# Optimization experiments

Measured on AMD Instinct MI355X. Metric: run time of the kernel, lower is better.

## Reference

```python
import jax, jax.numpy as jnp
import numpy as np

NUM_HEADS = 8
DIM_HEAD = 128
SCALE = DIM_HEAD ** -0.5


def setup_inputs() -> dict:
    key = jax.random.key(0)
    ks = jax.random.split(key, 6)
    B, N, D = 8, 1024, 1024
    return {
        "s_v": jax.random.normal(ks[0], (B, N, D), jnp.float32),
        "s_m": jax.random.normal(ks[1], (B, N, D), jnp.float32),
        "g_l": jax.random.normal(ks[2], (B, NUM_HEADS, N, N), jnp.float32),
        "W_qkv": jax.random.normal(ks[3], (D, 3 * NUM_HEADS * DIM_HEAD), jnp.float32) * (D ** -0.5),
        "W_qk": jax.random.normal(ks[4], (D, 2 * NUM_HEADS * DIM_HEAD), jnp.float32) * (D ** -0.5),
        "W_out": jax.random.normal(ks[5], (NUM_HEADS * DIM_HEAD, D), jnp.float32) * ((NUM_HEADS * DIM_HEAD) ** -0.5),
        "b_out": jnp.zeros((D,), jnp.float32),
    }


def _split_heads(t):
    # [b, n, h*d] -> [b, h, n, d]
    b, n, hd = t.shape
    return t.reshape(b, n, NUM_HEADS, DIM_HEAD).transpose(0, 2, 1, 3)


def reference(s_v, s_m, g_l, W_qkv, W_qk, W_out, b_out):
    b, n, _ = s_v.shape
    q_v, k_v, v = [_split_heads(t) for t in jnp.split(s_v @ W_qkv, 3, axis=-1)]
    q_m, k_m = [_split_heads(t) for t in jnp.split(s_m @ W_qk, 2, axis=-1)]
    # trajectory attention probs (softmaxed) times raw value-stream scores
    p_m = jax.nn.softmax(jnp.einsum('bhid,bhjd->bhij', q_m, k_m), axis=-1)
    p_v = jnp.einsum('bhid,bhjd->bhij', q_v, k_v)
    dots = p_m * p_v * SCALE + g_l
    attn = jax.nn.softmax(dots, axis=-1)
    out = jnp.einsum('bhij,bhjd->bhid', attn, v)
    out = out.transpose(0, 2, 1, 3).reshape(b, n, NUM_HEADS * DIM_HEAD)
    return out @ W_out + b_out
```

## Files before the change

kernel.cpp:

```cpp
#include <hip/hip_runtime.h>

typedef __attribute__((ext_vector_type(8))) short short8;
typedef __attribute__((ext_vector_type(8))) unsigned short ushortx8;
typedef __attribute__((ext_vector_type(4))) unsigned short ushortx4;
typedef __attribute__((ext_vector_type(4))) float floatx4;

#define SCALE_F 0.08838834764831845f

__device__ __forceinline__ float b2f(unsigned short u) {
  union { unsigned int u; float f; } c; c.u = ((unsigned int)u) << 16; return c.f;
}
__device__ __forceinline__ unsigned short f2b(float f) {
  union { float f; unsigned int u; } c; c.f = f;
  unsigned int u = c.u;
  u += 0x7fffu + ((u >> 16) & 1u);
  return (unsigned short)(u >> 16);
}

#define GLD_LDS16(g, l)                                              \
  __builtin_amdgcn_global_load_lds(                                  \
      (const __attribute__((address_space(1))) void*)(g),            \
      (__attribute__((address_space(3))) void*)(l), 16, 0, 0)

__global__ __launch_bounds__(256) void cast_bf16_kernel(
    const float* __restrict__ x, unsigned short* __restrict__ y, int n) {
  int i = (blockIdx.x * 256 + threadIdx.x) * 4;
  if (i >= n) return;
  float4 v = *(const float4*)(x + i);
  ushortx4 o;
  o[0] = f2b(v.x); o[1] = f2b(v.y); o[2] = f2b(v.z); o[3] = f2b(v.w);
  *(ushortx4*)(y + i) = o;
}

__global__ __launch_bounds__(256) void split3_kernel(
    const float* __restrict__ x, unsigned short* __restrict__ y) {
  int idx = blockIdx.x * 256 + threadIdx.x;
  int row = idx >> 8;
  int c4 = (idx & 255) * 4;
  float4 v = *(const float4*)(x + (size_t)row * 1024 + c4);
  ushortx4 hi, lo;
  hi[0] = f2b(v.x); lo[0] = f2b(v.x - b2f(hi[0]));
  hi[1] = f2b(v.y); lo[1] = f2b(v.y - b2f(hi[1]));
  hi[2] = f2b(v.z); lo[2] = f2b(v.z - b2f(hi[2]));
  hi[3] = f2b(v.w); lo[3] = f2b(v.w - b2f(hi[3]));
  unsigned short* yr = y + (size_t)row * 3072;
  *(ushortx4*)(yr + c4) = hi;
  *(ushortx4*)(yr + 1024 + c4) = lo;
  *(ushortx4*)(yr + 2048 + c4) = hi;
}

__global__ __launch_bounds__(256) void transpose_split_qk(
    const float* __restrict__ W, unsigned short* __restrict__ y) {
  __shared__ float tile[32][33];
  int t = threadIdx.x, tx = t & 31, ty = t >> 5;
  int n0 = blockIdx.x * 32, k0 = blockIdx.y * 32;
  for (int rr = ty; rr < 32; rr += 8)
    tile[rr][tx] = W[(size_t)(k0 + rr) * 2048 + n0 + tx];
  __syncthreads();
  for (int rr = ty; rr < 32; rr += 8) {
    float v = tile[tx][rr];
    unsigned short hi = f2b(v);
    unsigned short lo = f2b(v - b2f(hi));
    unsigned short* yr = y + (size_t)(n0 + rr) * 3072;
    yr[k0 + tx] = hi;
    yr[1024 + k0 + tx] = hi;
    yr[2048 + k0 + tx] = lo;
  }
}

template<int MODE>
__global__ __launch_bounds__(256) void transpose_any(
    const void* __restrict__ inv, void* __restrict__ outv,
    int R, int C, int ldin, int ldout,
    long sIb, long sIh, long sOb, long sOh, int pstart) {
  int z = blockIdx.z, p = pstart + z, b = p >> 3, h = p & 7;
  size_t ioff = (size_t)(sIb * b + sIh * h);
  size_t ooff = (size_t)(sOb * b + sOh * h);
  __shared__ float tile[32][33];
  int t = threadIdx.x, tx = t & 31, ty = t >> 5;
  int c0 = blockIdx.x * 32, r0 = blockIdx.y * 32;
  for (int rr = ty; rr < 32; rr += 8) {
    size_t idx = ioff + (size_t)(r0 + rr) * ldin + (c0 + tx);
    tile[rr][tx] = (MODE == 2) ? b2f(((const unsigned short*)inv)[idx])
                               : ((const float*)inv)[idx];
  }
  __syncthreads();
  for (int rr = ty; rr < 32; rr += 8) {
    size_t idx = ooff + (size_t)(c0 + rr) * ldout + (r0 + tx);
    ((unsigned short*)outv)[idx] = f2b(tile[tx][rr]);
  }
}

template<int OUT_BF16, int ADD_BIAS>
__global__ __launch_bounds__(256) void gemm128(
    const unsigned short* __restrict__ A, const unsigned short* __restrict__ BT,
    void* __restrict__ Cv, const float* __restrict__ bias,
    int K, int lda, int ldb, int ldc,
    long sAz, long sAb, long sAh, long sBz, long sBb, long sBh,
    long sCz, long sCb, long sCh, int pstart) {
  int z = blockIdx.z, p = pstart + z, bb = p >> 3, hh = p & 7;
  A  += (size_t)(sAz * z + sAb * bb + sAh * hh);
  BT += (size_t)(sBz * z + sBb * bb + sBh * hh);
  size_t coff = (size_t)(sCz * z + sCb * bb + sCh * hh);

  __shared__ unsigned short Al[128][32];
  __shared__ unsigned short Bl[128][32];
  int t = threadIdx.x;
  int m0 = blockIdx.y * 128, n0 = blockIdx.x * 128;
  int w = t >> 6, l = t & 63;
  int wm = (w >> 1) * 64, wn = (w & 1) * 64;
  int lrow = l & 15, lq = l >> 4;
  floatx4 acc[4][4] = {};

  int srow = t >> 2, scol = (t & 3) * 8;
  const unsigned short* ga = A + (size_t)(m0 + srow) * lda + scol;
  const unsigned short* gb = BT + (size_t)(n0 + srow) * ldb + scol;
  unsigned short* la = &Al[srow][scol];
  unsigned short* lb = &Bl[srow][scol];
  size_t lda64 = (size_t)64 * lda, ldb64 = (size_t)64 * ldb;

  for (int k0 = 0; k0 < K; k0 += 32) {
    GLD_LDS16(ga + k0, la);
    GLD_LDS16(ga + lda64 + k0, la + 64 * 32);
    GLD_LDS16(gb + k0, lb);
    GLD_LDS16(gb + ldb64 + k0, lb + 64 * 32);
    __syncthreads();
    short8 af[4], bf[4];
#pragma unroll
    for (int i = 0; i < 4; i++) af[i] = *(const short8*)&Al[wm + i * 16 + lrow][lq * 8];
#pragma unroll
    for (int j = 0; j < 4; j++) bf[j] = *(const short8*)&Bl[wn + j * 16 + lrow][lq * 8];
#pragma unroll
    for (int i = 0; i < 4; i++)
#pragma unroll
      for (int j = 0; j < 4; j++)
        acc[i][j] = __builtin_amdgcn_mfma_f32_16x16x32_bf16(af[i], bf[j], acc[i][j], 0, 0, 0);
    __syncthreads();
  }
#pragma unroll
  for (int i = 0; i < 4; i++)
#pragma unroll
    for (int j = 0; j < 4; j++)
#pragma unroll
      for (int r = 0; r < 4; r++) {
        int row = m0 + wm + i * 16 + lq * 4 + r;
        int col = n0 + wn + j * 16 + lrow;
        float v = acc[i][j][r];
        if (ADD_BIAS) v += bias[col];
        size_t idx = coff + (size_t)row * ldc + col;
        if (OUT_BF16) ((unsigned short*)Cv)[idx] = f2b(v);
        else          ((float*)Cv)[idx] = v;
      }
}

__global__ __launch_bounds__(256) void logits_prep(
    const float* __restrict__ qkf, unsigned short* __restrict__ qm,
    unsigned short* __restrict__ km, int pstart) {
  int idx = blockIdx.x * 256 + threadIdx.x;
  int z = blockIdx.y;
  int i = idx >> 5;
  int d4 = (idx & 31) * 4;
  int p = pstart + z, b = p >> 3, h = p & 7;
  const float* row = qkf + ((size_t)(b * 1024 + i)) * 2048 + h * 128;
  ushortx4 hi, lo;

  float4 q = *(const float4*)(row + d4);
  hi[0] = f2b(q.x); lo[0] = f2b(q.x - b2f(hi[0]));
  hi[1] = f2b(q.y); lo[1] = f2b(q.y - b2f(hi[1]));
  hi[2] = f2b(q.z); lo[2] = f2b(q.z - b2f(hi[2]));
  hi[3] = f2b(q.w); lo[3] = f2b(q.w - b2f(hi[3]));
  unsigned short* qr = qm + ((size_t)z * 1024 + i) * 384;
  *(ushortx4*)(qr + d4) = hi;
  *(ushortx4*)(qr + 128 + d4) = lo;
  *(ushortx4*)(qr + 256 + d4) = hi;

  float4 k = *(const float4*)(row + 1024 + d4);
  hi[0] = f2b(k.x); lo[0] = f2b(k.x - b2f(hi[0]));
  hi[1] = f2b(k.y); lo[1] = f2b(k.y - b2f(hi[1]));
  hi[2] = f2b(k.z); lo[2] = f2b(k.z - b2f(hi[2]));
  hi[3] = f2b(k.w); lo[3] = f2b(k.w - b2f(hi[3]));
  unsigned short* kr = km + ((size_t)z * 1024 + i) * 384;
  *(ushortx4*)(kr + d4) = hi;
  *(ushortx4*)(kr + 128 + d4) = hi;
  *(ushortx4*)(kr + 256 + d4) = lo;
}

__global__ __launch_bounds__(256) void softmax_combine(
    const float* __restrict__ smb, unsigned short* __restrict__ pvb,
    const float* __restrict__ g_l, int pstart) {
  int i = blockIdx.x, z = blockIdx.y;
  int p = pstart + z;
  const float* srow = smb + ((size_t)z * 1024 + i) * 1024;
  unsigned short* vrow = pvb + ((size_t)z * 1024 + i) * 1024;
  const float* grow = g_l + ((size_t)p * 1024 + i) * 1024;
  int t = threadIdx.x;
  __shared__ float red[4];

  float4 s = *(const float4*)(srow + t * 4);
  float mx = fmaxf(fmaxf(s.x, s.y), fmaxf(s.z, s.w));
#pragma unroll
  for (int o = 32; o; o >>= 1) mx = fmaxf(mx, __shfl_xor(mx, o));
  if ((t & 63) == 0) red[t >> 6] = mx;
  __syncthreads();
  mx = fmaxf(fmaxf(red[0], red[1]), fmaxf(red[2], red[3]));
  __syncthreads();
  float4 e;
  e.x = __expf(s.x - mx); e.y = __expf(s.y - mx);
  e.z = __expf(s.z - mx); e.w = __expf(s.w - mx);
  float sum = e.x + e.y + e.z + e.w;
#pragma unroll
  for (int o = 32; o; o >>= 1) sum += __shfl_xor(sum, o);
  if ((t & 63) == 0) red[t >> 6] = sum;
  __syncthreads();
  float inv = 1.0f / (red[0] + red[1] + red[2] + red[3]);
  __syncthreads();

  ushortx4 pv = *(const ushortx4*)(vrow + t * 4);
  float4 g = *(const float4*)(grow + t * 4);
  float4 d;
  d.x = e.x * inv * b2f(pv[0]) * SCALE_F + g.x;
  d.y = e.y * inv * b2f(pv[1]) * SCALE_F + g.y;
  d.z = e.z * inv * b2f(pv[2]) * SCALE_F + g.z;
  d.w = e.w * inv * b2f(pv[3]) * SCALE_F + g.w;

  float mx2 = fmaxf(fmaxf(d.x, d.y), fmaxf(d.z, d.w));
#pragma unroll
  for (int o = 32; o; o >>= 1) mx2 = fmaxf(mx2, __shfl_xor(mx2, o));
  if ((t & 63) == 0) red[t >> 6] = mx2;
  __syncthreads();
  mx2 = fmaxf(fmaxf(red[0], red[1]), fmaxf(red[2], red[3]));
  __syncthreads();
  float4 e2;
  e2.x = __expf(d.x - mx2); e2.y = __expf(d.y - mx2);
  e2.z = __expf(d.z - mx2); e2.w = __expf(d.w - mx2);
  float sum2 = e2.x + e2.y + e2.z + e2.w;
#pragma unroll
  for (int o = 32; o; o >>= 1) sum2 += __shfl_xor(sum2, o);
  if ((t & 63) == 0) red[t >> 6] = sum2;
  __syncthreads();
  float inv2 = 1.0f / (red[0] + red[1] + red[2] + red[3]);

  ushortx4 o4;
  o4[0] = f2b(e2.x * inv2); o4[1] = f2b(e2.y * inv2);
  o4[2] = f2b(e2.z * inv2); o4[3] = f2b(e2.w * inv2);
  *(ushortx4*)(vrow + t * 4) = o4;
}

extern "C" void kernel_launch(void* const* d_in, const int* in_sizes, int n_in,
                              void* d_out, int out_size, void* d_ws, size_t ws_size,
                              hipStream_t stream) {
  (void)in_sizes; (void)n_in; (void)out_size; (void)ws_size;
  const float* s_v   = (const float*)d_in[0];
  const float* s_m   = (const float*)d_in[1];
  const float* g_l   = (const float*)d_in[2];
  const float* W_qkv = (const float*)d_in[3];
  const float* W_qk  = (const float*)d_in[4];
  const float* W_out = (const float*)d_in[5];
  const float* b_out = (const float*)d_in[6];
  float* out = (float*)d_out;
  char* ws = (char*)d_ws;

  unsigned short* sv_bf  = (unsigned short*)(ws);
  unsigned short* qm384  = (unsigned short*)(ws);
  unsigned short* wtqkv  = (unsigned short*)(ws + 16777216);
  unsigned short* km384  = (unsigned short*)(ws + 16777216);
  unsigned short* wtout  = (unsigned short*)(ws + 29360128);
  unsigned short* qkvb   = (unsigned short*)(ws + 31457280);
  float*          qkf    = (float*)(ws + 81788928);
  unsigned short* vt     = (unsigned short*)(ws + 148897792);
  unsigned short* ao     = (unsigned short*)(ws + 165675008);
  unsigned short* smhl   = (unsigned short*)(ws + 182452224);
  float*          smb    = (float*)(ws + 182452224);
  unsigned short* wqk_hl = (unsigned short*)(ws + 249561088);
  unsigned short* pvb    = (unsigned short*)(ws + 249561088);

  cast_bf16_kernel<<<dim3(8192), 256, 0, stream>>>(s_v, sv_bf, 8388608);
  transpose_any<0><<<dim3(96, 32, 1), 256, 0, stream>>>(
      W_qkv, wtqkv, 1024, 3072, 3072, 1024, 0, 0, 0, 0, 0);
  transpose_any<0><<<dim3(32, 32, 1), 256, 0, stream>>>(
      W_out, wtout, 1024, 1024, 1024, 1024, 0, 0, 0, 0, 0);
  split3_kernel<<<dim3(8192), 256, 0, stream>>>(s_m, smhl);
  transpose_split_qk<<<dim3(64, 32, 1), 256, 0, stream>>>(W_qk, wqk_hl);
  gemm128<1, 0><<<dim3(24, 64, 1), 256, 0, stream>>>(
      sv_bf, wtqkv, qkvb, nullptr, 1024, 1024, 1024, 3072,
      0, 0, 0, 0, 0, 0, 0, 0, 0, 0);
  gemm128<0, 0><<<dim3(16, 64, 1), 256, 0, stream>>>(
      smhl, wqk_hl, qkf, nullptr, 3072, 3072, 3072, 2048,
      0, 0, 0, 0, 0, 0, 0, 0, 0, 0);
  transpose_any<2><<<dim3(4, 32, 64), 256, 0, stream>>>(
      qkvb + 2048, vt, 1024, 128, 3072, 1024,
      (long)1024 * 3072, 128, (long)1048576, 131072, 0);

  for (int c = 0; c < 4; c++) {
    int pstart = c * 16;
    logits_prep<<<dim3(128, 16), 256, 0, stream>>>(qkf, qm384, km384, pstart);
    gemm128<0, 0><<<dim3(8, 8, 16), 256, 0, stream>>>(
        qm384, km384, smb, nullptr, 384, 384, 384, 1024,
        (long)1024 * 384, 0, 0, (long)1024 * 384, 0, 0,
        (long)1048576, 0, 0, pstart);
    gemm128<1, 0><<<dim3(8, 8, 16), 256, 0, stream>>>(
        qkvb, qkvb + 1024, pvb, nullptr, 128, 3072, 3072, 1024,
        0, (long)1024 * 3072, 128, 0, (long)1024 * 3072, 128,
        (long)1048576, 0, 0, pstart);
    softmax_combine<<<dim3(1024, 16), 256, 0, stream>>>(smb, pvb, g_l, pstart);
    gemm128<1, 0><<<dim3(1, 8, 16), 256, 0, stream>>>(
        pvb, vt, ao, nullptr, 1024, 1024, 1024, 1024,
        (long)1048576, 0, 0, 0, (long)1048576, 131072,
        0, (long)1048576, 128, pstart);
  }
  gemm128<0, 1><<<dim3(8, 64, 1), 256, 0, stream>>>(
      ao, wtout, out, b_out, 1024, 1024, 1024, 1024,
      0, 0, 0, 0, 0, 0, 0, 0, 0, 0);
}
```

Baseline: 1.140 ms.

## Fuse value-stream QK, combine softmax and PV into flash-style kernel

Replaces three stages per chunk (the q_v·k_v GEMM writing a bf16 score matrix, the two-pass softmax_combine, and the attn·V GEMM) with a row_stats kernel plus one fused attn_pv kernel. attn_pv computes q_v·k_v tiles with MFMA, applies the precomputed trajectory softmax stats, adds g_l, runs an online softmax and accumulates P·V in registers. This removes the pvb round-trip through memory. The cost is a small grid (32x16 blocks of 256 threads), many syncthreads, and uncoalesced scalar loads of smb and g_l, which may hurt occupancy and bandwidth.

New measurement: 1.219 ms. +7.0%, slower.

```diff
diff --git a/kernel.cpp b/kernel.cpp
--- a/kernel.cpp
+++ b/kernel.cpp
@@ -185,65 +185,197 @@
   *(ushortx4*)(kr + 256 + d4) = lo;
 }
 
-__global__ __launch_bounds__(256) void softmax_combine(
-    const float* __restrict__ smb, unsigned short* __restrict__ pvb,
-    const float* __restrict__ g_l, int pstart) {
-  int i = blockIdx.x, z = blockIdx.y;
-  int p = pstart + z;
-  const float* srow = smb + ((size_t)z * 1024 + i) * 1024;
-  unsigned short* vrow = pvb + ((size_t)z * 1024 + i) * 1024;
-  const float* grow = g_l + ((size_t)p * 1024 + i) * 1024;
-  int t = threadIdx.x;
+__global__ __launch_bounds__(256) void row_stats(
+    const float* __restrict__ smb, float* __restrict__ mlb) {
+  int row = blockIdx.x, z = blockIdx.y, t = threadIdx.x;
+  const float* sr = smb + ((size_t)z * 1024 + row) * 1024;
   __shared__ float red[4];
-
-  float4 s = *(const float4*)(srow + t * 4);
-  float mx = fmaxf(fmaxf(s.x, s.y), fmaxf(s.z, s.w));
+  float4 v = *(const float4*)(sr + t * 4);
+  float mx = fmaxf(fmaxf(v.x, v.y), fmaxf(v.z, v.w));
 #pragma unroll
   for (int o = 32; o; o >>= 1) mx = fmaxf(mx, __shfl_xor(mx, o));
   if ((t & 63) == 0) red[t >> 6] = mx;
   __syncthreads();
   mx = fmaxf(fmaxf(red[0], red[1]), fmaxf(red[2], red[3]));
   __syncthreads();
-  float4 e;
-  e.x = __expf(s.x - mx); e.y = __expf(s.y - mx);
-  e.z = __expf(s.z - mx); e.w = __expf(s.w - mx);
-  float sum = e.x + e.y + e.z + e.w;
-#pragma unroll
-  for (int o = 32; o; o >>= 1) sum += __shfl_xor(sum, o);
-  if ((t & 63) == 0) red[t >> 6] = sum;
-  __syncthreads();
-  float inv = 1.0f / (red[0] + red[1] + red[2] + red[3]);
-  __syncthreads();
-
-  ushortx4 pv = *(const ushortx4*)(vrow + t * 4);
-  float4 g = *(const float4*)(grow + t * 4);
-  float4 d;
-  d.x = e.x * inv * b2f(pv[0]) * SCALE_F + g.x;
-  d.y = e.y * inv * b2f(pv[1]) * SCALE_F + g.y;
-  d.z = e.z * inv * b2f(pv[2]) * SCALE_F + g.z;
-  d.w = e.w * inv * b2f(pv[3]) * SCALE_F + g.w;
-
-  float mx2 = fmaxf(fmaxf(d.x, d.y), fmaxf(d.z, d.w));
-#pragma unroll
-  for (int o = 32; o; o >>= 1) mx2 = fmaxf(mx2, __shfl_xor(mx2, o));
-  if ((t & 63) == 0) red[t >> 6] = mx2;
-  __syncthreads();
-  mx2 = fmaxf(fmaxf(red[0], red[1]), fmaxf(red[2], red[3]));
-  __syncthreads();
-  float4 e2;
-  e2.x = __expf(d.x - mx2); e2.y = __expf(d.y - mx2);
-  e2.z = __expf(d.z - mx2); e2.w = __expf(d.w - mx2);
-  float sum2 = e2.x + e2.y + e2.z + e2.w;
-#pragma unroll
-  for (int o = 32; o; o >>= 1) sum2 += __shfl_xor(sum2, o);
-  if ((t & 63) == 0) red[t >> 6] = sum2;
-  __syncthreads();
-  float inv2 = 1.0f / (red[0] + red[1] + red[2] + red[3]);
-
-  ushortx4 o4;
-  o4[0] = f2b(e2.x * inv2); o4[1] = f2b(e2.y * inv2);
-  o4[2] = f2b(e2.z * inv2); o4[3] = f2b(e2.w * inv2);
-  *(ushortx4*)(vrow + t * 4) = o4;
+  float s = __expf(v.x - mx) + __expf(v.y - mx) + __expf(v.z - mx) + __expf(v.w - mx);
+#pragma unroll
+  for (int o = 32; o; o >>= 1) s += __shfl_xor(s, o);
+  if ((t & 63) == 0) red[t >> 6] = s;
+  __syncthreads();
+  if (t == 0) {
+    mlb[z * 2048 + row] = mx;
+    mlb[z * 2048 + 1024 + row] = red[0] + red[1] + red[2] + red[3];
+  }
+}
+
+__global__ __launch_bounds__(256) void attn_pv(
+    const unsigned short* __restrict__ qkv, const unsigned short* __restrict__ vt,
+    const float* __restrict__ smb, const float* __restrict__ mlb,
+    const float* __restrict__ g_l, unsigned short* __restrict__ ao, int pstart) {
+  int z = blockIdx.y, p = pstart + z, b = p >> 3, h = p & 7;
+  int r0 = blockIdx.x * 32;
+  int t = threadIdx.x, w = t >> 6, l = t & 63;
+  int lrow = l & 15, lq = l >> 4;
+  int wc = w * 32;
+  int sr = t >> 2, sc = (t & 3) * 8;
+
+  __shared__ unsigned short kvl[128][32];
+  __shared__ unsigned short vtl[128][32];
+  __shared__ unsigned short attnl[32][136];
+  __shared__ float mex[4][32];
+  __shared__ float lex[4][32];
+
+  short8 aq[4][2];
+#pragma unroll
+  for (int kc = 0; kc < 4; kc++)
+#pragma unroll
+    for (int i = 0; i < 2; i++)
+      aq[kc][i] = *(const short8*)(qkv +
+          (size_t)(b * 1024 + r0 + i * 16 + lrow) * 3072 + h * 128 + kc * 32 + lq * 8);
+
+  float Mr[8], Li[8];
+#pragma unroll
+  for (int i = 0; i < 2; i++)
+#pragma unroll
+    for (int r = 0; r < 4; r++) {
+      int rw = i * 16 + lq * 4 + r;
+      Mr[i * 4 + r] = mlb[z * 2048 + r0 + rw];
+      Li[i * 4 + r] = 1.0f / mlb[z * 2048 + 1024 + r0 + rw];
+    }
+
+  float m2[8], l2[8];
+#pragma unroll
+  for (int ri = 0; ri < 8; ri++) { m2[ri] = -1e30f; l2[ri] = 0.f; }
+  floatx4 Og[2][2] = {};
+
+  const size_t smrow0 = (size_t)z * 1024 + r0;
+  const size_t glrow0 = (size_t)p * 1024 + r0;
+  const size_t vbase = (size_t)p * 131072;
+  const size_t kvbase = (size_t)b * 1024 * 3072 + 1024 + h * 128;
+
+  for (int j0 = 0; j0 < 1024; j0 += 128) {
+    floatx4 pva[2][2] = {};
+#pragma unroll
+    for (int kc = 0; kc < 4; kc++) {
+      __syncthreads();
+      GLD_LDS16(qkv + kvbase + (size_t)(j0 + sr) * 3072 + kc * 32 + sc, &kvl[sr][sc]);
+      GLD_LDS16(qkv + kvbase + (size_t)(j0 + 64 + sr) * 3072 + kc * 32 + sc, &kvl[sr + 64][sc]);
+      __syncthreads();
+#pragma unroll
+      for (int i = 0; i < 2; i++)
+#pragma unroll
+        for (int jj = 0; jj < 2; jj++) {
+          short8 bf = *(const short8*)&kvl[wc + jj * 16 + lrow][lq * 8];
+          pva[i][jj] = __builtin_amdgcn_mfma_f32_16x16x32_bf16(aq[kc][i], bf, pva[i][jj], 0, 0, 0);
+        }
+    }
+    float dv[2][2][4];
+#pragma unroll
+    for (int i = 0; i < 2; i++)
+#pragma unroll
+      for (int r = 0; r < 4; r++) {
+        size_t ro = (smrow0 + i * 16 + lq * 4 + r) * 1024;
+        size_t go = (glrow0 + i * 16 + lq * 4 + r) * 1024;
+        float M = Mr[i * 4 + r], Lv = Li[i * 4 + r];
+#pragma unroll
+        for (int jj = 0; jj < 2; jj++) {
+          int col = j0 + wc + jj * 16 + lrow;
+          float sm = smb[ro + col];
+          float g = g_l[go + col];
+          float pm = __expf(sm - M) * Lv;
+          dv[i][jj][r] = pm * pva[i][jj][r] * SCALE_F + g;
+        }
+      }
+    float lmax[8];
+#pragma unroll
+    for (int i = 0; i < 2; i++)
+#pragma unroll
+      for (int r = 0; r < 4; r++) {
+        float m = fmaxf(dv[i][0][r], dv[i][1][r]);
+#pragma unroll
+        for (int o = 1; o < 16; o <<= 1) m = fmaxf(m, __shfl_xor(m, o));
+        lmax[i * 4 + r] = m;
+      }
+    if (lrow == 0) {
+#pragma unroll
+      for (int i = 0; i < 2; i++)
+#pragma unroll
+        for (int r = 0; r < 4; r++)
+          mex[w][i * 16 + lq * 4 + r] = lmax[i * 4 + r];
+    }
+    __syncthreads();
+    float alpha[8];
+#pragma unroll
+    for (int i = 0; i < 2; i++)
+#pragma unroll
+      for (int r = 0; r < 4; r++) {
+        int ri = i * 4 + r, rw = i * 16 + lq * 4 + r;
+        float mn = fmaxf(fmaxf(mex[0][rw], mex[1][rw]), fmaxf(mex[2][rw], mex[3][rw]));
+        mn = fmaxf(mn, m2[ri]);
+        alpha[ri] = __expf(m2[ri] - mn);
+        m2[ri] = mn;
+      }
+    float ev[2][2][4];
+#pragma unroll
+    for (int i = 0; i < 2; i++)
+#pragma unroll
+      for (int r = 0; r < 4; r++) {
+        int ri = i * 4 + r;
+        float e0 = __expf(dv[i][0][r] - m2[ri]);
+        float e1 = __expf(dv[i][1][r] - m2[ri]);
+        ev[i][0][r] = e0; ev[i][1][r] = e1;
+        float rs = e0 + e1;
+#pragma unroll
+        for (int o = 1; o < 16; o <<= 1) rs += __shfl_xor(rs, o);
+        l2[ri] = l2[ri] * alpha[ri] + rs;
+#pragma unroll
+        for (int jj = 0; jj < 2; jj++) Og[i][jj][r] *= alpha[ri];
+      }
+#pragma unroll
+    for (int i = 0; i < 2; i++)
+#pragma unroll
+      for (int jj = 0; jj < 2; jj++)
+#pragma unroll
+        for (int r = 0; r < 4; r++)
+          attnl[i * 16 + lq * 4 + r][wc + jj * 16 + lrow] = f2b(ev[i][jj][r]);
+    __syncthreads();
+#pragma unroll
+    for (int kc = 0; kc < 4; kc++) {
+      GLD_LDS16(vt + vbase + (size_t)sr * 1024 + j0 + kc * 32 + sc, &vtl[sr][sc]);
+      GLD_LDS16(vt + vbase + (size_t)(sr + 64) * 1024 + j0 + kc * 32 + sc, &vtl[sr + 64][sc]);
+      __syncthreads();
+#pragma unroll
+      for (int i = 0; i < 2; i++) {
+        short8 af = *(const short8*)&attnl[i * 16 + lrow][kc * 32 + lq * 8];
+#pragma unroll
+        for (int jj = 0; jj < 2; jj++) {
+          short8 bf = *(const short8*)&vtl[wc + jj * 16 + lrow][lq * 8];
+          Og[i][jj] = __builtin_amdgcn_mfma_f32_16x16x32_bf16(af, bf, Og[i][jj], 0, 0, 0);
+        }
+      }
+      if (kc < 3) __syncthreads();
+    }
+  }
+  if (lrow == 0) {
+#pragma unroll
+    for (int i = 0; i < 2; i++)
+#pragma unroll
+      for (int r = 0; r < 4; r++)
+        lex[w][i * 16 + lq * 4 + r] = l2[i * 4 + r];
+  }
+  __syncthreads();
+#pragma unroll
+  for (int i = 0; i < 2; i++)
+#pragma unroll
+    for (int r = 0; r < 4; r++) {
+      int rw = i * 16 + lq * 4 + r;
+      float inv = 1.0f / (lex[0][rw] + lex[1][rw] + lex[2][rw] + lex[3][rw]);
+#pragma unroll
+      for (int jj = 0; jj < 2; jj++)
+        ao[(size_t)(b * 1024 + r0 + rw) * 1024 + h * 128 + wc + jj * 16 + lrow] =
+            f2b(Og[i][jj][r] * inv);
+    }
 }
 
 extern "C" void kernel_launch(void* const* d_in, const int* in_sizes, int n_in,
@@ -272,7 +404,7 @@
   unsigned short* smhl   = (unsigned short*)(ws + 182452224);
   float*          smb    = (float*)(ws + 182452224);
   unsigned short* wqk_hl = (unsigned short*)(ws + 249561088);
-  unsigned short* pvb    = (unsigned short*)(ws + 249561088);
+  float*          mlb    = (float*)(ws + 249561088);
 
   cast_bf16_kernel<<<dim3(8192), 256, 0, stream>>>(s_v, sv_bf, 8388608);
   transpose_any<0><<<dim3(96, 32, 1), 256, 0, stream>>>(
@@ -298,15 +430,9 @@
         qm384, km384, smb, nullptr, 384, 384, 384, 1024,
         (long)1024 * 384, 0, 0, (long)1024 * 384, 0, 0,
         (long)1048576, 0, 0, pstart);
-    gemm128<1, 0><<<dim3(8, 8, 16), 256, 0, stream>>>(
-        qkvb, qkvb + 1024, pvb, nullptr, 128, 3072, 3072, 1024,
-        0, (long)1024 * 3072, 128, 0, (long)1024 * 3072, 128,
-        (long)1048576, 0, 0, pstart);
-    softmax_combine<<<dim3(1024, 16), 256, 0, stream>>>(smb, pvb, g_l, pstart);
-    gemm128<1, 0><<<dim3(1, 8, 16), 256, 0, stream>>>(
-        pvb, vt, ao, nullptr, 1024, 1024, 1024, 1024,
-        (long)1048576, 0, 0, 0, (long)1048576, 131072,
-        0, (long)1048576, 128, pstart);
+    row_stats<<<dim3(1024, 16), 256, 0, stream>>>(smb, mlb);
+    attn_pv<<<dim3(32, 16), 256, 0, stream>>>(
+        qkvb, vt, smb, mlb, g_l, ao, pstart);
   }
   gemm128<0, 1><<<dim3(8, 64, 1), 256, 0, stream>>>(
       ao, wtout, out, b_out, 1024, 1024, 1024, 1024,
```
